# Kernel optimization log

Measured on AMD Instinct MI355X. Metric: run time of the kernel, lower is better.

## Reference

```python
import jax, jax.numpy as jnp
import numpy as np

B, N = 32, 1000
HID, COM = 256, 64
T_LEN, NOP = 288, 3
NVAL, TP_D, CS_D, TIME_D = 9, 2, 4, 4
IN_C = CS_D + TP_D + NVAL            # 15, competition GAT input
IN_CO = IN_C + COM                    # 79, cooperation GAT input
OBS = TIME_D + TP_D + CS_D + 2 * COM + NVAL  # 147
K_D = K_F = 500                       # int(0.5*N + 0.5)
TEMP = 1.0
NEG = jnp.float32(-1e8)


def setup_inputs() -> dict:
    key = jax.random.key(0)
    ks = jax.random.split(key, 24)
    def nrm(k, shp, scale=0.05):
        return (jax.random.normal(k, shp, dtype=jnp.float32) * scale)
    return {
        "time_idx": jax.random.randint(ks[0], (B, N), 0, T_LEN, dtype=jnp.int32),
        "op_idx": jax.random.randint(ks[1], (B, N), 0, NOP, dtype=jnp.int32),
        "value_feats": jax.random.normal(ks[2], (B, N, NVAL), dtype=jnp.float32),
        "dpcs_mark": jax.random.randint(ks[3], (B, N, 1), 0, 2) > 0,
        "adj_comp": jax.random.randint(ks[4], (B, N, N), 0, 2) > 0,
        "adj_coop": jax.random.randint(ks[5], (B, N, N), 0, 2) > 0,
        "distance": jax.random.uniform(ks[6], (N, N), dtype=jnp.float32),
        "time_tab": jax.random.uniform(ks[7], (T_LEN, TIME_D), dtype=jnp.float32),
        "tp_tab": jax.random.uniform(ks[8], (NOP, TP_D), dtype=jnp.float32),
        "cs_tab": jax.random.uniform(ks[9], (N, CS_D), dtype=jnp.float32),
        "Wc": nrm(ks[10], (IN_C, COM)),
        "asrc_c": nrm(ks[11], (COM,)),
        "adst_c": nrm(ks[12], (COM,)),
        "wd_c": jnp.float32(0.1),
        "Wco": nrm(ks[13], (IN_CO, COM)),
        "asrc_co": nrm(ks[14], (COM,)),
        "adst_co": nrm(ks[15], (COM,)),
        "wd_co": jnp.float32(0.1),
        "Wp": nrm(ks[16], (OBS, HID)),
        "bp": jnp.zeros((HID,), dtype=jnp.float32),
        "vpd": nrm(ks[17], (HID,)),
        "vpf": nrm(ks[18], (HID,)),
    }


def gat(x, W, a_src, a_dst, w_d, adj, dist):
    """Single-head GAT over dense boolean adjacency. adj[b,j,i] True => edge j->i."""
    h = jnp.einsum("bnf,fd->bnd", x, W)                       # (B,N,D)
    e = (jnp.einsum("bid,d->bi", h, a_dst)[:, :, None]        # dst term
         + jnp.einsum("bjd,d->bj", h, a_src)[:, None, :]      # src term
         + w_d * dist.T[None])                                 # dist[j,i] edge feat
    e = jax.nn.leaky_relu(e, 0.2)
    mask = jnp.swapaxes(adj, 1, 2)                             # (B, dst i, src j)
    e = jnp.where(mask, e, NEG)
    alpha = jax.nn.softmax(e, axis=-1)
    alpha = jnp.where(mask, alpha, 0.0)                        # isolated nodes -> 0
    return jax.nn.elu(jnp.einsum("bij,bjd->bid", alpha, h))


def gated_pool(x_p, scores, valid, k, temp):
    scores = scores - scores.max(axis=1, keepdims=True)
    scores = jnp.where(valid, scores, NEG)                     # (B,N,1)
    val_topk = jax.lax.top_k(scores[..., 0], k)[0]             # (B,k)
    min_topk = val_topk.min(axis=-1)[:, None, None]
    scores = jnp.where(scores < min_topk, NEG, scores)
    w = jax.nn.softmax(scores / temp, axis=1)
    xg = x_p * w
    return jnp.concatenate([xg.sum(axis=1), xg.max(axis=1)], axis=-1)  # (B,2H)


def reference(time_idx, op_idx, value_feats, dpcs_mark, adj_comp, adj_coop,
              distance, time_tab, tp_tab, cs_tab, Wc, asrc_c, adst_c, wd_c,
              Wco, asrc_co, adst_co, wd_co, Wp, bp, vpd, vpf):
    time_e = time_tab[time_idx]                                # (B,N,4)
    tp_e = tp_tab[op_idx]                                      # (B,N,2)
    cs_e = jnp.broadcast_to(cs_tab[None], (B, N, CS_D))        # (B,N,4)
    vf_det = jax.lax.stop_gradient(value_feats)
    x = jnp.concatenate([cs_e, tp_e, vf_det], axis=-1)         # (B,N,15)
    comp_reps = gat(x, Wc, asrc_c, adst_c, wd_c, adj_comp, distance)
    x_m = jnp.concatenate([x, comp_reps], axis=-1)             # (B,N,79)
    coop_reps = gat(x_m, Wco, asrc_co, adst_co, wd_co, adj_coop, distance)
    sag = jnp.concatenate([time_e, cs_e, tp_e, value_feats, comp_reps, coop_reps], axis=-1)
    x_p = jnp.einsum("bnf,fh->bnh", sag, Wp) + bp              # (B,N,HID)
    scores_d = jnp.einsum("bnh,h->bn", x_p, vpd)[..., None]
    s_d = gated_pool(x_p, scores_d, dpcs_mark, K_D, TEMP)
    scores_f = jnp.einsum("bnh,h->bn", x_p, vpf)[..., None]
    s_f = gated_pool(x_p, scores_f, ~dpcs_mark, K_F, TEMP)
    return jnp.concatenate([s_f, s_d], axis=-1)                # (B, 4*HID)
```

## Files before the change

kernel.cpp:

```cpp
#include <hip/hip_runtime.h>
#include <hip/hip_bf16.h>

#define NB 32
#define NN 1000
#define COMD 64
#define HIDD 256
#define KSEL 500
#define TI 16
#define NSPL 32
#define ROWS 32
#define DSTRIDE 1024

typedef __hip_bfloat16 bf16;
typedef unsigned long long u64;
typedef __attribute__((ext_vector_type(4))) float f32x4;
typedef __attribute__((ext_vector_type(8))) short s16x8;
typedef __attribute__((ext_vector_type(4))) short s16x4;
typedef __attribute__((ext_vector_type(4))) unsigned short u16x4;
typedef __attribute__((ext_vector_type(2))) unsigned long long u64x2;

__device__ __forceinline__ float b2f(bf16 x){ return __bfloat162float(x); }

template<bool F32>
__device__ __forceinline__ float ldf(const void* p, long i){
  return F32 ? ((const float*)p)[i] : b2f(((const bf16*)p)[i]);
}
template<bool BINT>
__device__ __forceinline__ bool ldb(const void* p, long i){
  return BINT ? (((const int*)p)[i] != 0) : (((const unsigned char*)p)[i] != 0);
}

__device__ __forceinline__ float wave_sum(float v){
#pragma unroll
  for (int o = 32; o > 0; o >>= 1) v += __shfl_down(v, o, 64);
  return v;
}
__device__ __forceinline__ float wave_bsum(float v){
#pragma unroll
  for (int o = 32; o > 0; o >>= 1) v += __shfl_xor(v, o, 64);
  return v;
}
__device__ __forceinline__ float wave_bmax(float v){
#pragma unroll
  for (int o = 32; o > 0; o >>= 1) v = fmaxf(v, __shfl_xor(v, o, 64));
  return v;
}
__device__ __forceinline__ int wave_bsum_i(int v){
#pragma unroll
  for (int o = 32; o > 0; o >>= 1) v += __shfl_xor(v, o, 64);
  return v;
}
__device__ __forceinline__ unsigned fkey(float f){
  unsigned u = __float_as_uint(f);
  return (u & 0x80000000u) ? ~u : (u | 0x80000000u);
}
__device__ __forceinline__ void split_bf(float v, short& hi, short& lo){
  unsigned u = __float_as_uint(v);
  float hf = __uint_as_float(u & 0xFFFF0000u);
  hi = (short)(u >> 16);
  float r = v - hf;
  lo = (short)(__float_as_uint(r) >> 16);
}
__device__ __forceinline__ short f2bs(float v){
  bf16 h = __float2bfloat16(v);
  short s; __builtin_memcpy(&s, &h, 2); return s;
}
__device__ __forceinline__ void hB_write(short* hB_hi, short* hB_lo,
                                         int b, int n, int ch, float v){
  int kb = n >> 5, g4 = (n >> 3) & 3, u = n & 7;
  long off = ((((long)b * 32 + kb) * 4 + g4) * 64 + ch) * 8 + u;
  short hi, lo; split_bf(v, hi, lo);
  hB_hi[off] = hi; hB_lo[off] = lo;
}

__global__ void k_sniff(const void* dist, const void* adjc,
                        const void* wdc, const void* wdco,
                        int* flags, float* wd_out){
  if (blockIdx.x != 0 || threadIdx.x != 0) return;
  const unsigned* w = (const unsigned*)dist;
  int f32 = 0;
  for (int k = 0; k < 64; ++k) if ((w[k] & 0xFFFFu) >= 0x8000u){ f32 = 1; break; }
  const unsigned* bw = (const unsigned*)adjc;
  int as_int = 1;
  for (int k = 0; k < 64; ++k) if (bw[k] > 1u){ as_int = 0; break; }
  flags[0] = f32; flags[1] = as_int;
  wd_out[0] = f32 ? ((const float*)wdc)[0]  : b2f(((const bf16*)wdc)[0]);
  wd_out[1] = f32 ? ((const float*)wdco)[0] : b2f(((const bf16*)wdco)[0]);
}

template<bool F32>
__device__ __forceinline__ void dist_t_body(const void* dist, bf16* distTb){
  __shared__ bf16 tile[64][68];
  int t = threadIdx.x;
  int wv = t >> 6, lane = t & 63;
  int it = blockIdx.x * 64, jt = blockIdx.y * 64;
#pragma unroll
  for (int r = 0; r < 16; ++r){
    int jl = r * 4 + wv;
    int j = jt + jl, i = it + lane;
    float v = (j < NN && i < NN) ? ldf<F32>(dist, (long)j * NN + i) : 0.f;
    tile[jl][lane] = __float2bfloat16(v);
  }
  __syncthreads();
#pragma unroll
  for (int r = 0; r < 16; ++r){
    int il = r * 4 + wv;
    int i = it + il, j = jt + lane;
    if (i < NN) distTb[(long)i * DSTRIDE + j] = tile[lane][il];
  }
}
__global__ void k_dist_t(const int* flags, const void* dist, bf16* distTb){
  if (flags[0]) dist_t_body<true>(dist, distTb);
  else          dist_t_body<false>(dist, distTb);
}

template<bool BINT>
__device__ __forceinline__ void adjq_body(const void* adj, u64* adjQ){
  int t = threadIdx.x;
  int wv = t >> 6, lane = t & 63;
  int j0 = blockIdx.x * 64;
  int iw = blockIdx.y, b = blockIdx.z;
  long base = (long)b * NN * NN;
  int i = iw * 64 + lane;
  bool iok = i < NN;
#pragma unroll
  for (int r = 0; r < 16; ++r){
    int j = j0 + wv * 16 + r;
    bool pred = (iok && j < NN) ? ldb<BINT>(adj, base + (long)j * NN + i) : false;
    u64 word = __ballot(pred);
    if (lane == 0) adjQ[((long)b * 16 + iw) * 1024 + j] = word;
  }
}
__global__ void k_adjq(const int* flags, const void* adj, u64* adjQ){
  if (flags[1]) adjq_body<true>(adj, adjQ);
  else          adjq_body<false>(adj, adjQ);
}

template<bool F32>
__device__ __forceinline__ void wprep_body(
    const void* Wp, const void* vpd, const void* vpf, const void* bp,
    short* WpB_hi, short* WpB_lo, float* wv_ws){
  int f = blockIdx.x;
  int lane = threadIdx.x;
  if (f < 160){
    float wrow[4];
#pragma unroll
    for (int r = 0; r < 4; ++r){
      int ch = r * 64 + lane;
      wrow[r] = (f < 147) ? ldf<F32>(Wp, (long)f * HIDD + ch) : 0.f;
    }
    int kb = f >> 5, q = (f >> 3) & 3, u = f & 7;
#pragma unroll
    for (int r = 0; r < 4; ++r){
      int ch = r * 64 + lane;
      long off = (((long)(kb * 4 + q)) * 256 + ch) * 8 + u;
      short hi, lo; split_bf(wrow[r], hi, lo);
      WpB_hi[off] = hi; WpB_lo[off] = lo;
    }
    float ad = 0.f, af = 0.f;
#pragma unroll
    for (int r = 0; r < 4; ++r){
      int ch = r * 64 + lane;
      ad += wrow[r] * ldf<F32>(vpd, ch);
      af += wrow[r] * ldf<F32>(vpf, ch);
    }
    ad = wave_bsum(ad); af = wave_bsum(af);
    if (lane == 0){ wv_ws[f] = ad; wv_ws[160 + f] = af; }
  } else {
    float ad = 0.f, af = 0.f;
#pragma unroll
    for (int r = 0; r < 4; ++r){
      int ch = r * 64 + lane;
      float bb = ldf<F32>(bp, ch);
      ad += bb * ldf<F32>(vpd, ch);
      af += bb * ldf<F32>(vpf, ch);
    }
    ad = wave_bsum(ad); af = wave_bsum(af);
    if (lane == 0){ wv_ws[320] = ad; wv_ws[321] = af; }
  }
}
__global__ void k_wprep(const int* flags, const void* Wp, const void* vpd,
                        const void* vpf, const void* bp,
                        short* WpB_hi, short* WpB_lo, float* wv_ws){
  if (flags[0]) wprep_body<true >(Wp, vpd, vpf, bp, WpB_hi, WpB_lo, wv_ws);
  else          wprep_body<false>(Wp, vpd, vpf, bp, WpB_hi, WpB_lo, wv_ws);
}

template<bool F32>
__device__ __forceinline__ void embed_body(
    const int* op_idx, const void* vf, const void* cs_tab, const void* tp_tab,
    const void* Wc, const void* asrc, const void* adst,
    float* x_out, short* hB_hi, short* hB_lo, float* ed_out, float* es_out){
  int t = threadIdx.x;
  int w = t >> 6, lane = t & 63;
  int g = blockIdx.x * 4 + w;
  int b = g / NN, n = g - b * NN;
  int op = op_idx[g];
  float xv = 0.f, hacc = 0.f;
#pragma unroll
  for (int f = 0; f < 15; ++f){
    float x_f;
    if (f < 4)      x_f = ldf<F32>(cs_tab, n * 4 + f);
    else if (f < 6) x_f = ldf<F32>(tp_tab, op * 2 + (f - 4));
    else            x_f = ldf<F32>(vf, (long)g * 9 + (f - 6));
    if (lane == f) xv = x_f;
    hacc += x_f * ldf<F32>(Wc, f * COMD + lane);
  }
  if (lane < 15) x_out[g * 15 + lane] = xv;
  hB_write(hB_hi, hB_lo, b, n, lane, hacc);
  float sd = wave_sum(hacc * ldf<F32>(adst, lane));
  float ss = wave_sum(hacc * ldf<F32>(asrc, lane));
  if (lane == 0){ ed_out[g] = sd; es_out[g] = ss; }
}
__global__ void __launch_bounds__(256) k_embed(
    const int* flags, const int* op_idx, const void* vf, const void* cs_tab,
    const void* tp_tab, const void* Wc, const void* asrc, const void* adst,
    float* x_out, short* hB_hi, short* hB_lo, float* ed_out, float* es_out){
  if (flags[0]) embed_body<true >(op_idx, vf, cs_tab, tp_tab, Wc, asrc, adst, x_out, hB_hi, hB_lo, ed_out, es_out);
  else          embed_body<false>(op_idx, vf, cs_tab, tp_tab, Wc, asrc, adst, x_out, hB_hi, hB_lo, ed_out, es_out);
}

template<bool F32>
__device__ __forceinline__ void hco_body(
    const float* x_ws, const float* comp, const void* Wco,
    const void* asrc, const void* adst,
    short* hB_hi, short* hB_lo, float* ed_out, float* es_out){
  __shared__ float cx[4][80] __attribute__((aligned(16)));
  int t = threadIdx.x;
  int w = t >> 6, lane = t & 63;
  int base = blockIdx.x * 4;
  for (int idx = t; idx < 4 * 79; idx += 256){
    int nl = idx / 79, f = idx - nl * 79;
    int g = base + nl;
    cx[nl][f] = (f < 15) ? x_ws[g * 15 + f] : comp[(long)g * COMD + (f - 15)];
  }
  __syncthreads();
  int g = base + w;
  int b = g / NN, n = g - b * NN;
  float hacc = 0.f;
#pragma unroll
  for (int f4 = 0; f4 < 76; f4 += 4){
    float4 sv = *(const float4*)&cx[w][f4];
    float w0 = ldf<F32>(Wco, (f4 + 0) * COMD + lane);
    float w1 = ldf<F32>(Wco, (f4 + 1) * COMD + lane);
    float w2 = ldf<F32>(Wco, (f4 + 2) * COMD + lane);
    float w3 = ldf<F32>(Wco, (f4 + 3) * COMD + lane);
    hacc += sv.x * w0 + sv.y * w1 + sv.z * w2 + sv.w * w3;
  }
#pragma unroll
  for (int f = 76; f < 79; ++f)
    hacc += cx[w][f] * ldf<F32>(Wco, f * COMD + lane);
  hB_write(hB_hi, hB_lo, b, n, lane, hacc);
  float sd = wave_sum(hacc * ldf<F32>(adst, lane));
  float ss = wave_sum(hacc * ldf<F32>(asrc, lane));
  if (lane == 0){ ed_out[g] = sd; es_out[g] = ss; }
}
__global__ void __launch_bounds__(256) k_hco(
    const int* flags, const float* x_ws, const float* comp, const void* Wco,
    const void* asrc, const void* adst,
    short* hB_hi, short* hB_lo, float* ed_out, float* es_out){
  if (flags[0]) hco_body<true >(x_ws, comp, Wco, asrc, adst, hB_hi, hB_lo, ed_out, es_out);
  else          hco_body<false>(x_ws, comp, Wco, asrc, adst, hB_hi, hB_lo, ed_out, es_out);
}

__global__ void __launch_bounds__(256) k_gat(
    const float* __restrict__ ed, const float* __restrict__ es,
    const float* __restrict__ wd_ws, int wd_idx, const u64* __restrict__ adjQ,
    const bf16* __restrict__ distTb,
    const short* __restrict__ hB_hi, const short* __restrict__ hB_lo,
    float* __restrict__ reps){
  __shared__ short pA[32 * 544] __attribute__((aligned(16)));
  __shared__ float redz[TI][4];
  __shared__ float esred[4];
  int t = threadIdx.x;
  int wv = t >> 6, lane = t & 63;
  int b = blockIdx.y;
  int i0 = blockIdx.x * TI;
  float wd = wd_ws[wd_idx];
  int iw = i0 >> 6, sb = i0 & 63;
  int j0 = t * 4;

  const u64* aq = adjQ + ((long)b * 16 + iw) * 1024 + j0;
  u64x2 wA = *(const u64x2*)&aq[0];
  u64x2 wB = *(const u64x2*)&aq[2];
  unsigned wsh[4] = { (unsigned)(wA[0] >> sb), (unsigned)(wA[1] >> sb),
                      (unsigned)(wB[0] >> sb), (unsigned)(wB[1] >> sb) };
  float4 es4 = *(const float4*)&es[(long)b * NN + j0];
  float esv[4] = {es4.x, es4.y, es4.z, es4.w};
  float esm = -1e30f;
#pragma unroll
  for (int c = 0; c < 4; ++c)
    esm = fmaxf(esm, (j0 + c < NN) ? esv[c] : -1e30f);
  esm = wave_bmax(esm);
  if (lane == 0) esred[wv] = esm;

  float ed_i[TI]; float edm = -1e30f;
#pragma unroll
  for (int ti = 0; ti < TI; ++ti){
    int i = i0 + ti;
    float ev = ed[(long)b * NN + ((i < NN) ? i : (NN - 1))];
    ed_i[ti] = ev;
    edm = fmaxf(edm, (i < NN) ? ev : -1e30f);
  }
  __syncthreads();
  float M = fmaxf(fmaxf(esred[0], esred[1]), fmaxf(esred[2], esred[3]))
            + edm + fmaxf(wd, 0.f);
  M = fmaxf(M, 0.f);

  float p[TI][4];
  const bf16* dbase = distTb + j0;
#pragma unroll
  for (int ti = 0; ti < TI; ++ti){
    int i = i0 + ti;
    int ic = (i < NN) ? i : (NN - 1);
    u16x4 d4 = *(const u16x4*)&dbase[(long)ic * DSTRIDE];
    float edti = ed_i[ti];
#pragma unroll
    for (int c = 0; c < 4; ++c){
      float d = __uint_as_float((unsigned)d4[c] << 16);
      float v = edti + esv[c] + wd * d;
      v = fmaxf(v, 0.2f * v);
      bool edge = (wsh[c] >> ti) & 1u;
      float e = edge ? v : -1e30f;
      p[ti][c] = __expf(e - M);
    }
  }

  int kbw = 8 * wv + (lane >> 3);
  int qw = (lane >> 1) & 3;
  int u0 = 4 * (lane & 1);
  int wbase = kbw * 544 + qw * 136 + u0;
#pragma unroll
  for (int ti = 0; ti < TI; ++ti){
    float zs = p[ti][0] + p[ti][1] + p[ti][2] + p[ti][3];
    zs = wave_bsum(zs);
    if (lane == 0) redz[ti][wv] = zs;
    s16x4 s4 = { f2bs(p[ti][0]), f2bs(p[ti][1]), f2bs(p[ti][2]), f2bs(p[ti][3]) };
    *(s16x4*)&pA[wbase + ti * 8] = s4;
  }
  __syncthreads();

  int q = lane >> 4, m = lane & 15;
  int abase = q * 136 + m * 8;
  int ch = wv * 16 + m;
  const short* bh = hB_hi + (long)b * 65536 + ((long)q * 64 + ch) * 8;
  const short* bl = hB_lo + (long)b * 65536 + ((long)q * 64 + ch) * 8;
  f32x4 acc = {0.f, 0.f, 0.f, 0.f};
#pragma unroll
  for (int kb = 0; kb < 32; ++kb){
    s16x8 a   = *(const s16x8*)&pA[kb * 544 + abase];
    s16x8 bhi = *(const s16x8*)&bh[(long)kb * 2048];
    s16x8 blo = *(const s16x8*)&bl[(long)kb * 2048];
    acc = __builtin_amdgcn_mfma_f32_16x16x32_bf16(a, bhi, acc, 0, 0, 0);
    acc = __builtin_amdgcn_mfma_f32_16x16x32_bf16(a, blo, acc, 0, 0, 0);
  }
#pragma unroll
  for (int reg = 0; reg < 4; ++reg){
    int ti = (lane >> 4) * 4 + reg;
    float z = redz[ti][0] + redz[ti][1] + redz[ti][2] + redz[ti][3];
    float zi = (z > 0.f) ? 1.f / z : 0.f;
    float v = acc[reg] * zi;
    v = (v > 0.f) ? v : expm1f(v);
    int ch2 = wv * 16 + (lane & 15);
    if (i0 + ti < NN)
      reps[((long)b * NN + i0 + ti) * COMD + ch2] = v;
  }
}

template<bool F32>
__device__ __forceinline__ void xp_body(
    const int* time_idx, const int* op_idx, const void* vf, const void* time_tab,
    const void* cs_tab, const void* tp_tab, const float* comp, const float* coop,
    const short* __restrict__ WpB_hi, const short* __restrict__ WpB_lo,
    const float* __restrict__ wv_ws, const void* bp,
    float* x_p, float* scf, float* scd){
  __shared__ float sagF[16][148] __attribute__((aligned(16)));
  __shared__ short sagA_hi[5 * 16 * 40] __attribute__((aligned(16)));
  __shared__ short sagA_lo[5 * 16 * 40] __attribute__((aligned(16)));
  int t = threadIdx.x;
  int wv = t >> 6, lane = t & 63;
  int base = blockIdx.x * 16;

  for (int idx = t; idx < 16 * 147; idx += 256){
    int nl = idx / 147, f = idx - nl * 147;
    int g = base + nl;
    int n = g % NN;
    float v;
    if (f < 4)       v = ldf<F32>(time_tab, time_idx[g] * 4 + f);
    else if (f < 8)  v = ldf<F32>(cs_tab, n * 4 + (f - 4));
    else if (f < 10) v = ldf<F32>(tp_tab, op_idx[g] * 2 + (f - 8));
    else if (f < 19) v = ldf<F32>(vf, (long)g * 9 + (f - 10));
    else if (f < 83) v = comp[(long)g * COMD + (f - 19)];
    else             v = coop[(long)g * COMD + (f - 83)];
    sagF[nl][f] = v;
  }
  __syncthreads();

  for (int idx = t; idx < 16 * 160; idx += 256){
    int m = idx / 160, k = idx - m * 160;
    float v = (k < 147) ? sagF[m][k] : 0.f;
    int kb = k >> 5, q = (k >> 3) & 3, u = k & 7;
    short hi, lo; split_bf(v, hi, lo);
    int off = (kb * 16 + m) * 40 + q * 8 + u;
    sagA_hi[off] = hi; sagA_lo[off] = lo;
  }
  {
    int node = t >> 4, sub = t & 15;
    float ad = 0.f, af = 0.f;
    for (int f = sub; f < 147; f += 16){
      float s = sagF[node][f];
      ad += s * wv_ws[f];
      af += s * wv_ws[160 + f];
    }
#pragma unroll
    for (int o = 8; o > 0; o >>= 1){
      ad += __shfl_xor(ad, o, 64);
      af += __shfl_xor(af, o, 64);
    }
    if (sub == 0){
      scd[base + node] = ad + wv_ws[320];
      scf[base + node] = af + wv_ws[321];
    }
  }
  __syncthreads();

  int Ag = lane >> 4, Am = lane & 15;
  f32x4 acc[4] = {{0,0,0,0},{0,0,0,0},{0,0,0,0},{0,0,0,0}};
#pragma unroll
  for (int kb = 0; kb < 5; ++kb){
    int aoff = (kb * 16 + Am) * 40 + Ag * 8;
    s16x8 a_hi = *(const s16x8*)&sagA_hi[aoff];
    s16x8 a_lo = *(const s16x8*)&sagA_lo[aoff];
#pragma unroll
    for (int ct = 0; ct < 4; ++ct){
      int ch = wv * 64 + ct * 16 + Am;
      long boff = (((long)(kb * 4 + Ag)) * 256 + ch) * 8;
      s16x8 b_hi = *(const s16x8*)&WpB_hi[boff];
      s16x8 b_lo = *(const s16x8*)&WpB_lo[boff];
      acc[ct] = __builtin_amdgcn_mfma_f32_16x16x32_bf16(a_hi, b_hi, acc[ct], 0, 0, 0);
      acc[ct] = __builtin_amdgcn_mfma_f32_16x16x32_bf16(a_hi, b_lo, acc[ct], 0, 0, 0);
      acc[ct] = __builtin_amdgcn_mfma_f32_16x16x32_bf16(a_lo, b_hi, acc[ct], 0, 0, 0);
    }
  }
#pragma unroll
  for (int ct = 0; ct < 4; ++ct){
    int ch = wv * 64 + ct * 16 + (lane & 15);
    float bb = ldf<F32>(bp, ch);
#pragma unroll
    for (int reg = 0; reg < 4; ++reg){
      int row = (lane >> 4) * 4 + reg;
      x_p[(long)(base + row) * HIDD + ch] = acc[ct][reg] + bb;
    }
  }
}
__global__ void __launch_bounds__(256) k_xp(
    const int* flags, const int* time_idx, const int* op_idx, const void* vf,
    const void* time_tab, const void* cs_tab, const void* tp_tab,
    const float* comp, const float* coop,
    const short* WpB_hi, const short* WpB_lo, const float* wv_ws, const void* bp,
    float* x_p, float* scf, float* scd){
  if (flags[0]) xp_body<true >(time_idx, op_idx, vf, time_tab, cs_tab, tp_tab, comp, coop, WpB_hi, WpB_lo, wv_ws, bp, x_p, scf, scd);
  else          xp_body<false>(time_idx, op_idx, vf, time_tab, cs_tab, tp_tab, comp, coop, WpB_hi, WpB_lo, wv_ws, bp, x_p, scf, scd);
}

template<bool BINT>
__device__ __forceinline__ void topk_body(
    const float* scf, const float* scd, const void* mark, float* wls){
  int lane = threadIdx.x;
  int b = blockIdx.x, pool = blockIdx.y;
  const float* sc = (pool == 0) ? scf : scd;
  float v[16]; unsigned key[16];
  float m0 = -INFINITY;
#pragma unroll
  for (int r = 0; r < 16; ++r){
    int n = r * 64 + lane;
    float s = (n < NN) ? sc[b * NN + n] : -INFINITY;
    v[r] = s;
    m0 = fmaxf(m0, s);
  }
  m0 = wave_bmax(m0);
  float m1 = -INFINITY;
#pragma unroll
  for (int r = 0; r < 16; ++r){
    int n = r * 64 + lane;
    bool valid = false;
    if (n < NN){
      bool mk = ldb<BINT>(mark, b * NN + n);
      valid = (pool == 0) ? !mk : mk;
    }
    v[r] = valid ? (v[r] - m0) : -1e8f;
    key[r] = fkey(v[r]);
    if (n < NN) m1 = fmaxf(m1, v[r]);
  }
  m1 = wave_bmax(m1);

  unsigned lo = 0u, hi = 0xFFFFFFFFu;
  while (lo < hi){
    unsigned mid = lo + ((hi - lo) >> 1) + 1u;
    int c = 0;
#pragma unroll
    for (int r = 0; r < 16; ++r) c += (key[r] >= mid) ? 1 : 0;
    c = wave_bsum_i(c);
    if (c >= KSEL) lo = mid; else hi = mid - 1u;
  }

  float p[16];
  float ls = 0.f;
#pragma unroll
  for (int r = 0; r < 16; ++r){
    int n = r * 64 + lane;
    float pp = (n < NN && key[r] >= lo) ? __expf(v[r] - m1) : 0.f;
    p[r] = pp;
    ls += pp;
  }
  ls = wave_bsum(ls);
  float zinv = (ls > 0.f) ? 1.f / ls : 0.f;
  float* w_out = wls + ((long)b * 2 + pool) * 1024;
#pragma unroll
  for (int r = 0; r < 16; ++r){
    int n = r * 64 + lane;
    if (n < NN) w_out[n] = p[r] * zinv;
  }
}
__global__ void k_topk(const int* flags, const float* scf, const float* scd,
                       const void* mark, float* wls){
  if (flags[1]) topk_body<true >(scf, scd, mark, wls);
  else          topk_body<false>(scf, scd, mark, wls);
}

__global__ void __launch_bounds__(256) k_psum(
    const float* __restrict__ wls, const float* __restrict__ x_p,
    float* __restrict__ part){
  __shared__ float wf[ROWS], wdd[ROWS];
  int t = threadIdx.x;
  int b = blockIdx.x, z = blockIdx.y;
  int n0 = z * ROWS;
  int ns = min(ROWS, NN - n0);
  if (t < ns){
    wf[t]  = wls[((long)b * 2 + 0) * 1024 + n0 + t];
    wdd[t] = wls[((long)b * 2 + 1) * 1024 + n0 + t];
  }
  __syncthreads();
  float sf = 0.f, mf = -INFINITY, sd = 0.f, md = -INFINITY;
  const float* xb = x_p + ((long)b * NN + n0) * HIDD + t;
  for (int k = 0; k < ns; ++k){
    float xv = xb[(long)k * HIDD];
    float gf = wf[k] * xv;
    float gd = wdd[k] * xv;
    sf += gf; mf = fmaxf(mf, gf);
    sd += gd; md = fmaxf(md, gd);
  }
  long pb = (((long)b * NSPL + z) * 4) * HIDD + t;
  part[pb + 0 * HIDD] = sf;
  part[pb + 1 * HIDD] = mf;
  part[pb + 2 * HIDD] = sd;
  part[pb + 3 * HIDD] = md;
}

template<bool F32>
__device__ __forceinline__ void pfin_body(const float* part, void* out){
  int t = threadIdx.x;
  int b = blockIdx.x;
  float sf = 0.f, mf = -INFINITY, sd = 0.f, md = -INFINITY;
#pragma unroll
  for (int z = 0; z < NSPL; ++z){
    long pb = (((long)b * NSPL + z) * 4) * HIDD + t;
    sf += part[pb + 0 * HIDD];
    mf = fmaxf(mf, part[pb + 1 * HIDD]);
    sd += part[pb + 2 * HIDD];
    md = fmaxf(md, part[pb + 3 * HIDD]);
  }
  long ob = (long)b * 1024;
  if (F32){
    ((float*)out)[ob + t] = sf;
    ((float*)out)[ob + 256 + t] = mf;
    ((float*)out)[ob + 512 + t] = sd;
    ((float*)out)[ob + 768 + t] = md;
  } else {
    ((bf16*)out)[ob + t] = __float2bfloat16(sf);
    ((bf16*)out)[ob + 256 + t] = __float2bfloat16(mf);
    ((bf16*)out)[ob + 512 + t] = __float2bfloat16(sd);
    ((bf16*)out)[ob + 768 + t] = __float2bfloat16(md);
  }
}
__global__ void k_pfin(const int* flags, const float* part, void* out){
  if (flags[0]) pfin_body<true >(part, out);
  else          pfin_body<false>(part, out);
}

extern "C" void kernel_launch(void* const* d_in, const int* in_sizes, int n_in,
                              void* d_out, int out_size, void* d_ws, size_t ws_size,
                              hipStream_t stream){
  const int*  time_idx = (const int*)d_in[0];
  const int*  op_idx   = (const int*)d_in[1];
  const void* vfeat    = d_in[2];
  const void* dpcs     = d_in[3];
  const void* adj_comp = d_in[4];
  const void* adj_coop = d_in[5];
  const void* dist     = d_in[6];
  const void* time_tab = d_in[7];
  const void* tp_tab   = d_in[8];
  const void* cs_tab   = d_in[9];
  const void* Wc       = d_in[10];
  const void* asrc_c   = d_in[11];
  const void* adst_c   = d_in[12];
  const void* wd_c     = d_in[13];
  const void* Wco      = d_in[14];
  const void* asrc_co  = d_in[15];
  const void* adst_co  = d_in[16];
  const void* wd_co    = d_in[17];
  const void* Wp       = d_in[18];
  const void* bp       = d_in[19];
  const void* vpd      = d_in[20];
  const void* vpf      = d_in[21];

  char* ws = (char*)d_ws;
  size_t o = 0;
  auto alloc = [&](size_t bytes)->char*{
    char* p = ws + o; o = (o + bytes + 255) & ~(size_t)255; return p;
  };
  int*   flags  = (int*)alloc(16);
  float* wd_ws  = (float*)alloc(8);
  bf16*  distTb = (bf16*)alloc((size_t)NN * DSTRIDE * 2);
  u64*   adjQc  = (u64*)alloc((size_t)NB * 16 * 1024 * 8);
  u64*   adjQo  = (u64*)alloc((size_t)NB * 16 * 1024 * 8);
  float* x_ws   = (float*)alloc((size_t)NB * NN * 15 * 4);
  float* comp   = (float*)alloc((size_t)NB * NN * COMD * 4);
  float* coop   = (float*)alloc((size_t)NB * NN * COMD * 4);
  short* hB_hi  = (short*)alloc((size_t)NB * 65536 * 2);
  short* hB_lo  = (short*)alloc((size_t)NB * 65536 * 2);
  short* WpB_hi = (short*)alloc((size_t)5 * 4 * 256 * 8 * 2);
  short* WpB_lo = (short*)alloc((size_t)5 * 4 * 256 * 8 * 2);
  float* wv_ws  = (float*)alloc(322 * 4);
  float* ed_c   = (float*)alloc((size_t)NB * NN * 4 + 256);
  float* es_c   = (float*)alloc((size_t)NB * NN * 4 + 256);
  float* ed_o   = (float*)alloc((size_t)NB * NN * 4 + 256);
  float* es_o   = (float*)alloc((size_t)NB * NN * 4 + 256);
  float* scf    = (float*)alloc((size_t)NB * NN * 4);
  float* scd    = (float*)alloc((size_t)NB * NN * 4);
  float* wls    = (float*)alloc((size_t)NB * 2 * 1024 * 4);
  float* part   = (float*)alloc((size_t)NB * NSPL * 4 * HIDD * 4);
  float* x_p    = (float*)alloc((size_t)NB * NN * HIDD * 4);

  k_sniff<<<1, 64, 0, stream>>>(dist, adj_comp, wd_c, wd_co, flags, wd_ws);
  k_wprep<<<dim3(161), dim3(64), 0, stream>>>(flags, Wp, vpd, vpf, bp, WpB_hi, WpB_lo, wv_ws);
  k_dist_t<<<dim3(16, 16), dim3(256), 0, stream>>>(flags, dist, distTb);
  dim3 qg(16, 16, NB);
  k_adjq<<<qg, dim3(256), 0, stream>>>(flags, adj_comp, adjQc);
  k_adjq<<<qg, dim3(256), 0, stream>>>(flags, adj_coop, adjQo);
  k_embed<<<dim3(NB * NN / 4), dim3(256), 0, stream>>>(
      flags, op_idx, vfeat, cs_tab, tp_tab, Wc, asrc_c, adst_c,
      x_ws, hB_hi, hB_lo, ed_c, es_c);
  k_gat<<<dim3((NN + TI - 1) / TI, NB), dim3(256), 0, stream>>>(
      ed_c, es_c, wd_ws, 0, adjQc, distTb, hB_hi, hB_lo, comp);
  k_hco<<<dim3(NB * NN / 4), dim3(256), 0, stream>>>(
      flags, x_ws, comp, Wco, asrc_co, adst_co, hB_hi, hB_lo, ed_o, es_o);
  k_gat<<<dim3((NN + TI - 1) / TI, NB), dim3(256), 0, stream>>>(
      ed_o, es_o, wd_ws, 1, adjQo, distTb, hB_hi, hB_lo, coop);
  k_xp<<<dim3(NB * NN / 16), dim3(256), 0, stream>>>(
      flags, time_idx, op_idx, vfeat, time_tab, cs_tab, tp_tab, comp, coop,
      WpB_hi, WpB_lo, wv_ws, bp, x_p, scf, scd);
  k_topk<<<dim3(NB, 2), dim3(64), 0, stream>>>(flags, scf, scd, dpcs, wls);
  k_psum<<<dim3(NB, NSPL), dim3(256), 0, stream>>>(wls, x_p, part);
  k_pfin<<<dim3(NB), dim3(256), 0, stream>>>(flags, part, d_out);
}
```

Baseline: 545.8 us.

## Fuse prep kernels, compute per-batch source max via atomics, MFMA cooperation projection

Merges the sniff, weight prep, distance transpose and both adjacency bit-pack kernels into one role-dispatched prep kernel, which cuts launches and serial dependencies. The per-batch maximum of the source attention term is now gathered with atomicMax in the embed and hco kernels, so the GAT kernel no longer does a block reduction and barrier to find it. The cooperation projection is rewritten as a split-bf16 MFMA GEMM over 16-node tiles. Its attention dot products use vectors folded into Wco ahead of time. The changes add global atomics and a precision split whose accuracy should match the old fp32 path.

```diff
diff --git a/kernel.cpp b/kernel.cpp
--- a/kernel.cpp
+++ b/kernel.cpp
@@ -11,6 +11,14 @@
 #define ROWS 32
 #define DSTRIDE 1024
 
+#define PB_DT   0
+#define PB_AQ1  256
+#define PB_AQ2  8448
+#define PB_WP   16640
+#define PB_WCO  16680
+#define PB_MISC 16704
+#define PB_N    16705
+
 typedef __hip_bfloat16 bf16;
 typedef unsigned long long u64;
 typedef __attribute__((ext_vector_type(4))) float f32x4;
@@ -54,6 +62,10 @@
   unsigned u = __float_as_uint(f);
   return (u & 0x80000000u) ? ~u : (u | 0x80000000u);
 }
+__device__ __forceinline__ float unfkey(unsigned k){
+  unsigned u = (k & 0x80000000u) ? (k ^ 0x80000000u) : ~k;
+  return __uint_as_float(u);
+}
 __device__ __forceinline__ void split_bf(float v, short& hi, short& lo){
   unsigned u = __float_as_uint(v);
   float hf = __uint_as_float(u & 0xFFFF0000u);
@@ -72,28 +84,20 @@
   short hi, lo; split_bf(v, hi, lo);
   hB_hi[off] = hi; hB_lo[off] = lo;
 }
-
-__global__ void k_sniff(const void* dist, const void* adjc,
-                        const void* wdc, const void* wdco,
-                        int* flags, float* wd_out){
-  if (blockIdx.x != 0 || threadIdx.x != 0) return;
-  const unsigned* w = (const unsigned*)dist;
-  int f32 = 0;
-  for (int k = 0; k < 64; ++k) if ((w[k] & 0xFFFFu) >= 0x8000u){ f32 = 1; break; }
-  const unsigned* bw = (const unsigned*)adjc;
-  int as_int = 1;
-  for (int k = 0; k < 64; ++k) if (bw[k] > 1u){ as_int = 0; break; }
-  flags[0] = f32; flags[1] = as_int;
-  wd_out[0] = f32 ? ((const float*)wdc)[0]  : b2f(((const bf16*)wdc)[0]);
-  wd_out[1] = f32 ? ((const float*)wdco)[0] : b2f(((const bf16*)wdco)[0]);
+__device__ __forceinline__ void sniff2(const void* dist, const void* adjc,
+                                       int lane, int& f32, int& as_int){
+  unsigned wdist = ((const unsigned*)dist)[lane];
+  unsigned wadj  = ((const unsigned*)adjc)[lane];
+  f32 = (__ballot((wdist & 0xFFFFu) >= 0x8000u) != 0ull) ? 1 : 0;
+  as_int = (__ballot(wadj > 1u) == 0ull) ? 1 : 0;
 }
 
 template<bool F32>
-__device__ __forceinline__ void dist_t_body(const void* dist, bf16* distTb){
+__device__ void dist_t_role(const void* dist, bf16* distTb, int rel){
   __shared__ bf16 tile[64][68];
   int t = threadIdx.x;
   int wv = t >> 6, lane = t & 63;
-  int it = blockIdx.x * 64, jt = blockIdx.y * 64;
+  int it = (rel & 15) * 64, jt = (rel >> 4) * 64;
 #pragma unroll
   for (int r = 0; r < 16; ++r){
     int jl = r * 4 + wv;
@@ -109,17 +113,12 @@
     if (i < NN) distTb[(long)i * DSTRIDE + j] = tile[lane][il];
   }
 }
-__global__ void k_dist_t(const int* flags, const void* dist, bf16* distTb){
-  if (flags[0]) dist_t_body<true>(dist, distTb);
-  else          dist_t_body<false>(dist, distTb);
-}
-
 template<bool BINT>
-__device__ __forceinline__ void adjq_body(const void* adj, u64* adjQ){
+__device__ void adjq_role(const void* adj, u64* adjQ, int rel){
   int t = threadIdx.x;
   int wv = t >> 6, lane = t & 63;
-  int j0 = blockIdx.x * 64;
-  int iw = blockIdx.y, b = blockIdx.z;
+  int j0 = (rel & 15) * 64;
+  int iw = (rel >> 4) & 15, b = rel >> 8;
   long base = (long)b * NN * NN;
   int i = iw * 64 + lane;
   bool iok = i < NN;
@@ -131,66 +130,114 @@
     if (lane == 0) adjQ[((long)b * 16 + iw) * 1024 + j] = word;
   }
 }
-__global__ void k_adjq(const int* flags, const void* adj, u64* adjQ){
-  if (flags[1]) adjq_body<true>(adj, adjQ);
-  else          adjq_body<false>(adj, adjQ);
-}
-
 template<bool F32>
-__device__ __forceinline__ void wprep_body(
+__device__ void wp_role(const void* Wp, const void* vpd, const void* vpf,
+                        short* WpB_hi, short* WpB_lo, float* wv_ws, int rel){
+  int t = threadIdx.x;
+  int g = t >> 6, lane = t & 63;
+  int f = rel * 4 + g;
+  float wrow[4];
+#pragma unroll
+  for (int r = 0; r < 4; ++r){
+    int ch = r * 64 + lane;
+    wrow[r] = (f < 147) ? ldf<F32>(Wp, (long)f * HIDD + ch) : 0.f;
+  }
+  int kb = f >> 5, q = (f >> 3) & 3, u = f & 7;
+#pragma unroll
+  for (int r = 0; r < 4; ++r){
+    int ch = r * 64 + lane;
+    long off = (((long)(kb * 4 + q)) * 256 + ch) * 8 + u;
+    short hi, lo; split_bf(wrow[r], hi, lo);
+    WpB_hi[off] = hi; WpB_lo[off] = lo;
+  }
+  float ad = 0.f, af = 0.f;
+#pragma unroll
+  for (int r = 0; r < 4; ++r){
+    int ch = r * 64 + lane;
+    ad += wrow[r] * ldf<F32>(vpd, ch);
+    af += wrow[r] * ldf<F32>(vpf, ch);
+  }
+  ad = wave_bsum(ad); af = wave_bsum(af);
+  if (lane == 0){ wv_ws[f] = ad; wv_ws[160 + f] = af; }
+}
+template<bool F32>
+__device__ void wco_role(const void* Wco, const void* asrc, const void* adst,
+                         short* WcoB_hi, short* WcoB_lo, float* pvco, int rel){
+  int t = threadIdx.x;
+  int g = t >> 6, lane = t & 63;
+  int f = rel * 4 + g;
+  float w = (f < 79) ? ldf<F32>(Wco, (long)f * COMD + lane) : 0.f;
+  int kb = f >> 5, q = (f >> 3) & 3, u = f & 7;
+  long off = (((long)(kb * 4 + q)) * 64 + lane) * 8 + u;
+  short hi, lo; split_bf(w, hi, lo);
+  WcoB_hi[off] = hi; WcoB_lo[off] = lo;
+  float dd = wave_bsum(w * ldf<F32>(adst, lane));
+  float ss = wave_bsum(w * ldf<F32>(asrc, lane));
+  if (lane == 0){ pvco[f] = dd; pvco[96 + f] = ss; }
+}
+template<bool F32>
+__device__ void misc_role(const void* wdc, const void* wdco,
+                          const void* bp, const void* vpd, const void* vpf,
+                          int f32, int as_int,
+                          int* flags, float* wd_ws, float* wv_ws, unsigned* esmax_u){
+  int t = threadIdx.x;
+  if (t < 64) esmax_u[t] = 0u;
+  if (t >= 64) return;
+  int lane = t;
+  float ad = 0.f, af = 0.f;
+#pragma unroll
+  for (int r = 0; r < 4; ++r){
+    int ch = r * 64 + lane;
+    float bb = ldf<F32>(bp, ch);
+    ad += bb * ldf<F32>(vpd, ch);
+    af += bb * ldf<F32>(vpf, ch);
+  }
+  ad = wave_bsum(ad); af = wave_bsum(af);
+  if (lane == 0){
+    wv_ws[320] = ad; wv_ws[321] = af;
+    wd_ws[0] = ldf<F32>(wdc, 0);
+    wd_ws[1] = ldf<F32>(wdco, 0);
+    flags[0] = f32; flags[1] = as_int;
+  }
+}
+__global__ void __launch_bounds__(256) k_prep(
+    const void* dist, const void* adj_comp, const void* adj_coop,
+    const void* wdc, const void* wdco,
     const void* Wp, const void* vpd, const void* vpf, const void* bp,
-    short* WpB_hi, short* WpB_lo, float* wv_ws){
-  int f = blockIdx.x;
-  int lane = threadIdx.x;
-  if (f < 160){
-    float wrow[4];
-#pragma unroll
-    for (int r = 0; r < 4; ++r){
-      int ch = r * 64 + lane;
-      wrow[r] = (f < 147) ? ldf<F32>(Wp, (long)f * HIDD + ch) : 0.f;
-    }
-    int kb = f >> 5, q = (f >> 3) & 3, u = f & 7;
-#pragma unroll
-    for (int r = 0; r < 4; ++r){
-      int ch = r * 64 + lane;
-      long off = (((long)(kb * 4 + q)) * 256 + ch) * 8 + u;
-      short hi, lo; split_bf(wrow[r], hi, lo);
-      WpB_hi[off] = hi; WpB_lo[off] = lo;
-    }
-    float ad = 0.f, af = 0.f;
-#pragma unroll
-    for (int r = 0; r < 4; ++r){
-      int ch = r * 64 + lane;
-      ad += wrow[r] * ldf<F32>(vpd, ch);
-      af += wrow[r] * ldf<F32>(vpf, ch);
-    }
-    ad = wave_bsum(ad); af = wave_bsum(af);
-    if (lane == 0){ wv_ws[f] = ad; wv_ws[160 + f] = af; }
+    const void* Wco, const void* asrc_co, const void* adst_co,
+    int* flags, float* wd_ws, bf16* distTb, u64* adjQc, u64* adjQo,
+    short* WpB_hi, short* WpB_lo, float* wv_ws,
+    short* WcoB_hi, short* WcoB_lo, float* pvco, unsigned* esmax_u){
+  int blk = blockIdx.x;
+  int f32, as_int;
+  sniff2(dist, adj_comp, threadIdx.x & 63, f32, as_int);
+  if (blk < PB_AQ1){
+    if (f32) dist_t_role<true >(dist, distTb, blk);
+    else     dist_t_role<false>(dist, distTb, blk);
+  } else if (blk < PB_AQ2){
+    if (as_int) adjq_role<true >(adj_comp, adjQc, blk - PB_AQ1);
+    else        adjq_role<false>(adj_comp, adjQc, blk - PB_AQ1);
+  } else if (blk < PB_WP){
+    if (as_int) adjq_role<true >(adj_coop, adjQo, blk - PB_AQ2);
+    else        adjq_role<false>(adj_coop, adjQo, blk - PB_AQ2);
+  } else if (blk < PB_WCO){
+    if (f32) wp_role<true >(Wp, vpd, vpf, WpB_hi, WpB_lo, wv_ws, blk - PB_WP);
+    else     wp_role<false>(Wp, vpd, vpf, WpB_hi, WpB_lo, wv_ws, blk - PB_WP);
+  } else if (blk < PB_MISC){
+    if (f32) wco_role<true >(Wco, asrc_co, adst_co, WcoB_hi, WcoB_lo, pvco, blk - PB_WCO);
+    else     wco_role<false>(Wco, asrc_co, adst_co, WcoB_hi, WcoB_lo, pvco, blk - PB_WCO);
   } else {
-    float ad = 0.f, af = 0.f;
-#pragma unroll
-    for (int r = 0; r < 4; ++r){
-      int ch = r * 64 + lane;
-      float bb = ldf<F32>(bp, ch);
-      ad += bb * ldf<F32>(vpd, ch);
-      af += bb * ldf<F32>(vpf, ch);
-    }
-    ad = wave_bsum(ad); af = wave_bsum(af);
-    if (lane == 0){ wv_ws[320] = ad; wv_ws[321] = af; }
-  }
-}
-__global__ void k_wprep(const int* flags, const void* Wp, const void* vpd,
-                        const void* vpf, const void* bp,
-                        short* WpB_hi, short* WpB_lo, float* wv_ws){
-  if (flags[0]) wprep_body<true >(Wp, vpd, vpf, bp, WpB_hi, WpB_lo, wv_ws);
-  else          wprep_body<false>(Wp, vpd, vpf, bp, WpB_hi, WpB_lo, wv_ws);
+    if (f32) misc_role<true >(wdc, wdco, bp, vpd, vpf, f32, as_int, flags, wd_ws, wv_ws, esmax_u);
+    else     misc_role<false>(wdc, wdco, bp, vpd, vpf, f32, as_int, flags, wd_ws, wv_ws, esmax_u);
+  }
 }
 
 template<bool F32>
 __device__ __forceinline__ void embed_body(
     const int* op_idx, const void* vf, const void* cs_tab, const void* tp_tab,
     const void* Wc, const void* asrc, const void* adst,
-    float* x_out, short* hB_hi, short* hB_lo, float* ed_out, float* es_out){
+    float* x_out, short* hB_hi, short* hB_lo, float* ed_out, float* es_out,
+    unsigned* esmax_u){
   int t = threadIdx.x;
   int w = t >> 6, lane = t & 63;
   int g = blockIdx.x * 4 + w;
@@ -210,57 +257,87 @@
   hB_write(hB_hi, hB_lo, b, n, lane, hacc);
   float sd = wave_sum(hacc * ldf<F32>(adst, lane));
   float ss = wave_sum(hacc * ldf<F32>(asrc, lane));
-  if (lane == 0){ ed_out[g] = sd; es_out[g] = ss; }
+  if (lane == 0){
+    ed_out[g] = sd; es_out[g] = ss;
+    atomicMax(&esmax_u[b], fkey(ss));
+  }
 }
 __global__ void __launch_bounds__(256) k_embed(
     const int* flags, const int* op_idx, const void* vf, const void* cs_tab,
     const void* tp_tab, const void* Wc, const void* asrc, const void* adst,
-    float* x_out, short* hB_hi, short* hB_lo, float* ed_out, float* es_out){
-  if (flags[0]) embed_body<true >(op_idx, vf, cs_tab, tp_tab, Wc, asrc, adst, x_out, hB_hi, hB_lo, ed_out, es_out);
-  else          embed_body<false>(op_idx, vf, cs_tab, tp_tab, Wc, asrc, adst, x_out, hB_hi, hB_lo, ed_out, es_out);
-}
-
-template<bool F32>
-__device__ __forceinline__ void hco_body(
-    const float* x_ws, const float* comp, const void* Wco,
-    const void* asrc, const void* adst,
-    short* hB_hi, short* hB_lo, float* ed_out, float* es_out){
-  __shared__ float cx[4][80] __attribute__((aligned(16)));
-  int t = threadIdx.x;
-  int w = t >> 6, lane = t & 63;
-  int base = blockIdx.x * 4;
-  for (int idx = t; idx < 4 * 79; idx += 256){
+    float* x_out, short* hB_hi, short* hB_lo, float* ed_out, float* es_out,
+    unsigned* esmax_u){
+  if (flags[0]) embed_body<true >(op_idx, vf, cs_tab, tp_tab, Wc, asrc, adst, x_out, hB_hi, hB_lo, ed_out, es_out, esmax_u);
+  else          embed_body<false>(op_idx, vf, cs_tab, tp_tab, Wc, asrc, adst, x_out, hB_hi, hB_lo, ed_out, es_out, esmax_u);
+}
+
+__global__ void __launch_bounds__(256) k_hco(
+    const float* __restrict__ x_ws, const float* __restrict__ comp,
+    const short* __restrict__ WcoB_hi, const short* __restrict__ WcoB_lo,
+    const float* __restrict__ pvco,
+    short* hB_hi, short* hB_lo, float* ed_out, float* es_out, unsigned* esmax_u){
+  __shared__ float cx[16][80] __attribute__((aligned(16)));
+  __shared__ short cA_hi[3 * 16 * 40] __attribute__((aligned(16)));
+  __shared__ short cA_lo[3 * 16 * 40] __attribute__((aligned(16)));
+  int t = threadIdx.x;
+  int wv = t >> 6, lane = t & 63;
+  int base = blockIdx.x * 16;
+  for (int idx = t; idx < 16 * 79; idx += 256){
     int nl = idx / 79, f = idx - nl * 79;
     int g = base + nl;
     cx[nl][f] = (f < 15) ? x_ws[g * 15 + f] : comp[(long)g * COMD + (f - 15)];
   }
   __syncthreads();
-  int g = base + w;
-  int b = g / NN, n = g - b * NN;
-  float hacc = 0.f;
-#pragma unroll
-  for (int f4 = 0; f4 < 76; f4 += 4){
-    float4 sv = *(const float4*)&cx[w][f4];
-    float w0 = ldf<F32>(Wco, (f4 + 0) * COMD + lane);
-    float w1 = ldf<F32>(Wco, (f4 + 1) * COMD + lane);
-    float w2 = ldf<F32>(Wco, (f4 + 2) * COMD + lane);
-    float w3 = ldf<F32>(Wco, (f4 + 3) * COMD + lane);
-    hacc += sv.x * w0 + sv.y * w1 + sv.z * w2 + sv.w * w3;
-  }
-#pragma unroll
-  for (int f = 76; f < 79; ++f)
-    hacc += cx[w][f] * ldf<F32>(Wco, f * COMD + lane);
-  hB_write(hB_hi, hB_lo, b, n, lane, hacc);
-  float sd = wave_sum(hacc * ldf<F32>(adst, lane));
-  float ss = wave_sum(hacc * ldf<F32>(asrc, lane));
-  if (lane == 0){ ed_out[g] = sd; es_out[g] = ss; }
-}
-__global__ void __launch_bounds__(256) k_hco(
-    const int* flags, const float* x_ws, const float* comp, const void* Wco,
-    const void* asrc, const void* adst,
-    short* hB_hi, short* hB_lo, float* ed_out, float* es_out){
-  if (flags[0]) hco_body<true >(x_ws, comp, Wco, asrc, adst, hB_hi, hB_lo, ed_out, es_out);
-  else          hco_body<false>(x_ws, comp, Wco, asrc, adst, hB_hi, hB_lo, ed_out, es_out);
+  {
+    int node = t >> 4, sub = t & 15;
+    float dd = 0.f, ss = 0.f;
+    for (int f = sub; f < 79; f += 16){
+      float c = cx[node][f];
+      dd += c * pvco[f];
+      ss += c * pvco[96 + f];
+    }
+#pragma unroll
+    for (int o = 8; o > 0; o >>= 1){
+      dd += __shfl_xor(dd, o, 64);
+      ss += __shfl_xor(ss, o, 64);
+    }
+    if (sub == 0){
+      int g = base + node;
+      ed_out[g] = dd; es_out[g] = ss;
+      atomicMax(&esmax_u[g / NN], fkey(ss));
+    }
+  }
+  for (int idx = t; idx < 16 * 96; idx += 256){
+    int m = idx / 96, k = idx - m * 96;
+    float v = (k < 79) ? cx[m][k] : 0.f;
+    int kb = k >> 5, q = (k >> 3) & 3, u = k & 7;
+    short hi, lo; split_bf(v, hi, lo);
+    int off = (kb * 16 + m) * 40 + q * 8 + u;
+    cA_hi[off] = hi; cA_lo[off] = lo;
+  }
+  __syncthreads();
+  int q = lane >> 4, m = lane & 15;
+  int ch = wv * 16 + m;
+  f32x4 acc = {0.f, 0.f, 0.f, 0.f};
+#pragma unroll
+  for (int kb = 0; kb < 3; ++kb){
+    int aoff = (kb * 16 + m) * 40 + q * 8;
+    s16x8 a_hi = *(const s16x8*)&cA_hi[aoff];
+    s16x8 a_lo = *(const s16x8*)&cA_lo[aoff];
+    long boff = (((long)(kb * 4 + q)) * 64 + ch) * 8;
+    s16x8 b_hi = *(const s16x8*)&WcoB_hi[boff];
+    s16x8 b_lo = *(const s16x8*)&WcoB_lo[boff];
+    acc = __builtin_amdgcn_mfma_f32_16x16x32_bf16(a_hi, b_hi, acc, 0, 0, 0);
+    acc = __builtin_amdgcn_mfma_f32_16x16x32_bf16(a_hi, b_lo, acc, 0, 0, 0);
+    acc = __builtin_amdgcn_mfma_f32_16x16x32_bf16(a_lo, b_hi, acc, 0, 0, 0);
+  }
+#pragma unroll
+  for (int reg = 0; reg < 4; ++reg){
+    int row = (lane >> 4) * 4 + reg;
+    int g = base + row;
+    int b = g / NN, n = g - b * NN;
+    hB_write(hB_hi, hB_lo, b, n, ch, acc[reg]);
+  }
 }
 
 __global__ void __launch_bounds__(256) k_gat(
@@ -268,10 +345,10 @@
     const float* __restrict__ wd_ws, int wd_idx, const u64* __restrict__ adjQ,
     const bf16* __restrict__ distTb,
     const short* __restrict__ hB_hi, const short* __restrict__ hB_lo,
+    const unsigned* __restrict__ esmax_u,
     float* __restrict__ reps){
   __shared__ short pA[32 * 544] __attribute__((aligned(16)));
   __shared__ float redz[TI][4];
-  __shared__ float esred[4];
   int t = threadIdx.x;
   int wv = t >> 6, lane = t & 63;
   int b = blockIdx.y;
@@ -287,12 +364,6 @@
                       (unsigned)(wB[0] >> sb), (unsigned)(wB[1] >> sb) };
   float4 es4 = *(const float4*)&es[(long)b * NN + j0];
   float esv[4] = {es4.x, es4.y, es4.z, es4.w};
-  float esm = -1e30f;
-#pragma unroll
-  for (int c = 0; c < 4; ++c)
-    esm = fmaxf(esm, (j0 + c < NN) ? esv[c] : -1e30f);
-  esm = wave_bmax(esm);
-  if (lane == 0) esred[wv] = esm;
 
   float ed_i[TI]; float edm = -1e30f;
 #pragma unroll
@@ -302,9 +373,7 @@
     ed_i[ti] = ev;
     edm = fmaxf(edm, (i < NN) ? ev : -1e30f);
   }
-  __syncthreads();
-  float M = fmaxf(fmaxf(esred[0], esred[1]), fmaxf(esred[2], esred[3]))
-            + edm + fmaxf(wd, 0.f);
+  float M = edm + unfkey(esmax_u[b]) + fmaxf(wd, 0.f);
   M = fmaxf(M, 0.f);
 
   float p[TI][4];
@@ -619,44 +688,47 @@
   auto alloc = [&](size_t bytes)->char*{
     char* p = ws + o; o = (o + bytes + 255) & ~(size_t)255; return p;
   };
-  int*   flags  = (int*)alloc(16);
-  float* wd_ws  = (float*)alloc(8);
-  bf16*  distTb = (bf16*)alloc((size_t)NN * DSTRIDE * 2);
-  u64*   adjQc  = (u64*)alloc((size_t)NB * 16 * 1024 * 8);
-  u64*   adjQo  = (u64*)alloc((size_t)NB * 16 * 1024 * 8);
-  float* x_ws   = (float*)alloc((size_t)NB * NN * 15 * 4);
-  float* comp   = (float*)alloc((size_t)NB * NN * COMD * 4);
-  float* coop   = (float*)alloc((size_t)NB * NN * COMD * 4);
-  short* hB_hi  = (short*)alloc((size_t)NB * 65536 * 2);
-  short* hB_lo  = (short*)alloc((size_t)NB * 65536 * 2);
-  short* WpB_hi = (short*)alloc((size_t)5 * 4 * 256 * 8 * 2);
-  short* WpB_lo = (short*)alloc((size_t)5 * 4 * 256 * 8 * 2);
-  float* wv_ws  = (float*)alloc(322 * 4);
-  float* ed_c   = (float*)alloc((size_t)NB * NN * 4 + 256);
-  float* es_c   = (float*)alloc((size_t)NB * NN * 4 + 256);
-  float* ed_o   = (float*)alloc((size_t)NB * NN * 4 + 256);
-  float* es_o   = (float*)alloc((size_t)NB * NN * 4 + 256);
-  float* scf    = (float*)alloc((size_t)NB * NN * 4);
-  float* scd    = (float*)alloc((size_t)NB * NN * 4);
-  float* wls    = (float*)alloc((size_t)NB * 2 * 1024 * 4);
-  float* part   = (float*)alloc((size_t)NB * NSPL * 4 * HIDD * 4);
-  float* x_p    = (float*)alloc((size_t)NB * NN * HIDD * 4);
-
-  k_sniff<<<1, 64, 0, stream>>>(dist, adj_comp, wd_c, wd_co, flags, wd_ws);
-  k_wprep<<<dim3(161), dim3(64), 0, stream>>>(flags, Wp, vpd, vpf, bp, WpB_hi, WpB_lo, wv_ws);
-  k_dist_t<<<dim3(16, 16), dim3(256), 0, stream>>>(flags, dist, distTb);
-  dim3 qg(16, 16, NB);
-  k_adjq<<<qg, dim3(256), 0, stream>>>(flags, adj_comp, adjQc);
-  k_adjq<<<qg, dim3(256), 0, stream>>>(flags, adj_coop, adjQo);
+  int*      flags   = (int*)alloc(16);
+  float*    wd_ws   = (float*)alloc(8);
+  unsigned* esmax_u = (unsigned*)alloc(64 * 4);
+  bf16*  distTb  = (bf16*)alloc((size_t)NN * DSTRIDE * 2);
+  u64*   adjQc   = (u64*)alloc((size_t)NB * 16 * 1024 * 8);
+  u64*   adjQo   = (u64*)alloc((size_t)NB * 16 * 1024 * 8);
+  float* x_ws    = (float*)alloc((size_t)NB * NN * 15 * 4);
+  float* comp    = (float*)alloc((size_t)NB * NN * COMD * 4);
+  float* coop    = (float*)alloc((size_t)NB * NN * COMD * 4);
+  short* hB_hi   = (short*)alloc((size_t)NB * 65536 * 2);
+  short* hB_lo   = (short*)alloc((size_t)NB * 65536 * 2);
+  short* WpB_hi  = (short*)alloc((size_t)5 * 4 * 256 * 8 * 2);
+  short* WpB_lo  = (short*)alloc((size_t)5 * 4 * 256 * 8 * 2);
+  short* WcoB_hi = (short*)alloc((size_t)3 * 4 * 64 * 8 * 2);
+  short* WcoB_lo = (short*)alloc((size_t)3 * 4 * 64 * 8 * 2);
+  float* wv_ws   = (float*)alloc(322 * 4);
+  float* pvco    = (float*)alloc(192 * 4);
+  float* ed_c    = (float*)alloc((size_t)NB * NN * 4 + 256);
+  float* es_c    = (float*)alloc((size_t)NB * NN * 4 + 256);
+  float* ed_o    = (float*)alloc((size_t)NB * NN * 4 + 256);
+  float* es_o    = (float*)alloc((size_t)NB * NN * 4 + 256);
+  float* scf     = (float*)alloc((size_t)NB * NN * 4);
+  float* scd     = (float*)alloc((size_t)NB * NN * 4);
+  float* wls     = (float*)alloc((size_t)NB * 2 * 1024 * 4);
+  float* part    = (float*)alloc((size_t)NB * NSPL * 4 * HIDD * 4);
+  float* x_p     = (float*)alloc((size_t)NB * NN * HIDD * 4);
+
+  k_prep<<<dim3(PB_N), dim3(256), 0, stream>>>(
+      dist, adj_comp, adj_coop, wd_c, wd_co, Wp, vpd, vpf, bp,
+      Wco, asrc_co, adst_co,
+      flags, wd_ws, distTb, adjQc, adjQo, WpB_hi, WpB_lo, wv_ws,
+      WcoB_hi, WcoB_lo, pvco, esmax_u);
   k_embed<<<dim3(NB * NN / 4), dim3(256), 0, stream>>>(
       flags, op_idx, vfeat, cs_tab, tp_tab, Wc, asrc_c, adst_c,
-      x_ws, hB_hi, hB_lo, ed_c, es_c);
+      x_ws, hB_hi, hB_lo, ed_c, es_c, esmax_u);
   k_gat<<<dim3((NN + TI - 1) / TI, NB), dim3(256), 0, stream>>>(
-      ed_c, es_c, wd_ws, 0, adjQc, distTb, hB_hi, hB_lo, comp);
-  k_hco<<<dim3(NB * NN / 4), dim3(256), 0, stream>>>(
-      flags, x_ws, comp, Wco, asrc_co, adst_co, hB_hi, hB_lo, ed_o, es_o);
+      ed_c, es_c, wd_ws, 0, adjQc, distTb, hB_hi, hB_lo, esmax_u, comp);
+  k_hco<<<dim3(NB * NN / 16), dim3(256), 0, stream>>>(
+      x_ws, comp, WcoB_hi, WcoB_lo, pvco, hB_hi, hB_lo, ed_o, es_o, esmax_u + NB);
   k_gat<<<dim3((NN + TI - 1) / TI, NB), dim3(256), 0, stream>>>(
-      ed_o, es_o, wd_ws, 1, adjQo, distTb, hB_hi, hB_lo, coop);
+      ed_o, es_o, wd_ws, 1, adjQo, distTb, hB_hi, hB_lo, esmax_u + NB, coop);
   k_xp<<<dim3(NB * NN / 16), dim3(256), 0, stream>>>(
       flags, time_idx, op_idx, vfeat, time_tab, cs_tab, tp_tab, comp, coop,
       WpB_hi, WpB_lo, wv_ws, bp, x_p, scf, scd);
```

After: 1.028 ms. +88.4%, slower.
